# Kernel optimization log

Hardware: AMD Instinct MI355X
Metric: run time of the kernel (lower is better)

## Reference

```python
import jax, jax.numpy as jnp
import numpy as np

BITS = 4
MAXQ = (1 << BITS) - 1  # 15
GROUPSIZE = 128
IN_F = 8192
OUT_F = 8192
PACK = 32 // BITS  # 8 values per int32


def setup_inputs() -> dict:
    key = jax.random.key(0)
    k_x, k_w, k_z, k_s, k_b = jax.random.split(key, 5)
    groups = IN_F // GROUPSIZE
    x = jax.random.normal(k_x, (4, 32, IN_F), dtype=jnp.float32)
    # bit-packed int32 weight / zeros (random bit patterns are valid quantized data)
    qweight = jax.random.randint(k_w, (IN_F // PACK, OUT_F), 0, 2**31 - 1, dtype=jnp.int32)
    qzeros = jax.random.randint(k_z, (groups, OUT_F // PACK), 0, 2**31 - 1, dtype=jnp.int32)
    scales = (jax.random.uniform(k_s, (groups, OUT_F), dtype=jnp.float32) * 0.01 + 1e-3)
    g_idx = (jnp.arange(IN_F, dtype=jnp.int32) // GROUPSIZE).astype(jnp.int32)
    bias = jax.random.normal(k_b, (OUT_F,), dtype=jnp.float32) * 0.01
    return {"x": x, "qweight": qweight, "qzeros": qzeros, "scales": scales,
            "g_idx": g_idx, "bias": bias}


def _dequant(qweight, qzeros, scales, g_idx):
    shifts = jnp.arange(0, 32, BITS, dtype=jnp.int32)  # [PACK]
    # unpack weights along the input dim: [in/PACK, PACK, out] -> [in, out]
    w = (qweight[:, None, :] >> shifts[None, :, None]) & MAXQ
    w = w.reshape(-1, qweight.shape[1])
    # unpack zeros along the output dim: [groups, out/PACK, PACK] -> [groups, out]
    # GPTQ stores (zero - 1), so add 1 back
    z = ((qzeros[:, :, None] >> shifts[None, None, :]) & MAXQ) + 1
    z = z.reshape(qzeros.shape[0], -1)
    # per-group dequant: W[i, o] = scales[g_idx[i], o] * (w[i, o] - z[g_idx[i], o])
    W = scales[g_idx] * (w.astype(scales.dtype) - z[g_idx].astype(scales.dtype))
    return W  # [in, out]


def reference(x, qweight, qzeros, scales, g_idx, bias):
    W = _dequant(qweight, qzeros, scales, g_idx)
    out = jnp.einsum('bsi,io->bso', x, W) + bias
    return out
```

## Files before the change

### kernel.cpp

```cpp
#include <hip/hip_runtime.h>
#include <hip/hip_bf16.h>
#include <stdint.h>


#define IN_F 8192
#define OUT_F 8192
#define MROWS 128
#define KSPLIT 8
#define KCHUNK (IN_F / KSPLIT)
#define BN 64
#define BK 64

typedef short short8_t __attribute__((ext_vector_type(8)));
typedef float float4_t __attribute__((ext_vector_type(4)));

__device__ __forceinline__ void gl_lds16(const void* g, void* l) {
  auto g1 = (const __attribute__((address_space(1))) unsigned int*)((uintptr_t)g);
  auto l3 = (__attribute__((address_space(3))) unsigned int*)((uintptr_t)l);
  __builtin_amdgcn_global_load_lds(g1, l3, 16, 0, 0);
}

__global__ void cvt_x(const float* __restrict__ x, unsigned short* __restrict__ xb) {
  const int i = (blockIdx.x * 256 + threadIdx.x) * 8;
  float4_t a = *(const float4_t*)(x + i);
  float4_t b = *(const float4_t*)(x + i + 4);
  union { short8_t v; __hip_bfloat162 h[4]; } u;
  u.h[0] = __float22bfloat162_rn(make_float2(a.x, a.y));
  u.h[1] = __float22bfloat162_rn(make_float2(a.z, a.w));
  u.h[2] = __float22bfloat162_rn(make_float2(b.x, b.y));
  u.h[3] = __float22bfloat162_rn(make_float2(b.z, b.w));
  *(short8_t*)(xb + i) = u.v;
}

__global__ void init_out(float* __restrict__ out, const float* __restrict__ bias) {
  const int i = (blockIdx.x * 256 + threadIdx.x) * 4;
  const int o = i & (OUT_F - 1);
  *(float4_t*)(out + i) = *(const float4_t*)(bias + o);
}

__global__ __launch_bounds__(256, 4) void gptq_gemm(
    const unsigned short* __restrict__ xb,
    const int* __restrict__ qweight,
    const int* __restrict__ qzeros,
    const float* __restrict__ scales,
    float* __restrict__ out)
{
  __shared__ unsigned short As[MROWS * BK];
  __shared__ unsigned short Bs[BN * BK];

  const int tid  = threadIdx.x;
  const int lane = tid & 63;
  const int wv   = tid >> 6;
  const int wm   = (wv >> 1) * 64;
  const int wn   = (wv & 1) * 32;

  const int o0  = blockIdx.x * BN;
  const int kc0 = blockIdx.y * KCHUNK;

  const int a_kb = (lane & 7) ^ (lane >> 3);

  const int u = tid & 31;
  const int r = tid >> 5;

  float4_t acc[4][2];
  const float4_t z4 = {0.f, 0.f, 0.f, 0.f};
#pragma unroll
  for (int i = 0; i < 4; ++i)
#pragma unroll
    for (int j = 0; j < 2; ++j) acc[i][j] = z4;

  float sc[2], zs[2];
  {
    const int g = kc0 >> 7;
#pragma unroll
    for (int oi = 0; oi < 2; ++oi) {
      const int o = o0 + u + 32 * oi;
      sc[oi] = scales[g * OUT_F + o];
      const int zp = qzeros[g * (OUT_F / 8) + (o >> 3)];
      zs[oi] = sc[oi] * (float)(((zp >> (4 * (o & 7))) & 15) + 1);
    }
  }
  int qw[2];
  {
    const int kp = kc0 >> 3;
    qw[0] = qweight[(size_t)(kp + r) * OUT_F + o0 + u];
    qw[1] = qweight[(size_t)(kp + r) * OUT_F + o0 + u + 32];
  }

#pragma unroll 2
  for (int it = 0; it < KCHUNK / BK; ++it) {
    const int k0 = kc0 + it * BK;

#pragma unroll
    for (int inst = 0; inst < 4; ++inst) {
      const int mrow = wv * 32 + inst * 8 + (lane >> 3);
      gl_lds16(xb + (size_t)mrow * IN_F + k0 + a_kb * 8,
               (void*)(As + wv * 2048 + inst * 512));
    }

#pragma unroll
    for (int oi = 0; oi < 2; ++oi) {
      const int n = u + 32 * oi;
      union { short8_t v; __hip_bfloat162 h[4]; } bw;
#pragma unroll
      for (int jj = 0; jj < 4; ++jj) {
        const int w0 = (qw[oi] >> (8 * jj)) & 15;
        const int w1 = (qw[oi] >> (8 * jj + 4)) & 15;
        bw.h[jj] = __float22bfloat162_rn(make_float2(
            (float)w0 * sc[oi] - zs[oi], (float)w1 * sc[oi] - zs[oi]));
      }
      *(short8_t*)(Bs + n * BK + (r ^ (n & 7)) * 8) = bw.v;
    }

    __syncthreads();

    {
      const int itn = (it + 1 < KCHUNK / BK) ? it + 1 : it;
      const int kp = (kc0 + itn * BK) >> 3;
      qw[0] = qweight[(size_t)(kp + r) * OUT_F + o0 + u];
      qw[1] = qweight[(size_t)(kp + r) * OUT_F + o0 + u + 32];
      if ((((it + 1) & 1) == 0) && (it + 1 < KCHUNK / BK)) {
        const int g = (kc0 + (it + 1) * BK) >> 7;
#pragma unroll
        for (int oi = 0; oi < 2; ++oi) {
          const int o = o0 + u + 32 * oi;
          sc[oi] = scales[g * OUT_F + o];
          const int zp = qzeros[g * (OUT_F / 8) + (o >> 3)];
          zs[oi] = sc[oi] * (float)(((zp >> (4 * (o & 7))) & 15) + 1);
        }
      }
    }

#pragma unroll
    for (int ks = 0; ks < 2; ++ks) {
      const int c = ks * 4 + (lane >> 4);
      const int pos8 = (c ^ (lane & 7)) * 8;
      const int l15 = lane & 15;
      short8_t af[4], bf[2];
#pragma unroll
      for (int t = 0; t < 4; ++t)
        af[t] = *(const short8_t*)(As + (wm + t * 16 + l15) * BK + pos8);
#pragma unroll
      for (int t = 0; t < 2; ++t)
        bf[t] = *(const short8_t*)(Bs + (wn + t * 16 + l15) * BK + pos8);
#pragma unroll
      for (int mt = 0; mt < 4; ++mt)
#pragma unroll
        for (int nt = 0; nt < 2; ++nt)
          acc[mt][nt] = __builtin_amdgcn_mfma_f32_16x16x32_bf16(
              af[mt], bf[nt], acc[mt][nt], 0, 0, 0);
    }

    __syncthreads();
  }

  const int row4 = (lane >> 4) * 4;
  const int col = lane & 15;
#pragma unroll
  for (int mt = 0; mt < 4; ++mt)
#pragma unroll
    for (int nt = 0; nt < 2; ++nt)
#pragma unroll
      for (int rr = 0; rr < 4; ++rr) {
        const int m = wm + mt * 16 + row4 + rr;
        const int o = o0 + wn + nt * 16 + col;
        atomicAdd(out + (size_t)m * OUT_F + o, acc[mt][nt][rr]);
      }
}

extern "C" void kernel_launch(void* const* d_in, const int* in_sizes, int n_in,
                              void* d_out, int out_size, void* d_ws, size_t ws_size,
                              hipStream_t stream) {
  const float* x        = (const float*)d_in[0];
  const int*   qweight  = (const int*)d_in[1];
  const int*   qzeros   = (const int*)d_in[2];
  const float* scales   = (const float*)d_in[3];
  const float* bias     = (const float*)d_in[5];
  float* out = (float*)d_out;
  unsigned short* xb = (unsigned short*)d_ws;

  cvt_x<<<dim3((MROWS * IN_F) / (256 * 8)), 256, 0, stream>>>(x, xb);
  init_out<<<dim3((MROWS * OUT_F) / (256 * 4)), 256, 0, stream>>>(out, bias);
  gptq_gemm<<<dim3(OUT_F / BN, KSPLIT), 256, 0, stream>>>(xb, qweight, qzeros, scales, out);
}
```

Baseline: 130.0 us.

## Dequantize weights directly into MFMA B-fragments in registers, dropping B LDS tile

Each wave now loads its own packed weights in MFMA fragment order and dequantizes them straight into registers, so the B shared-memory tile and its store/load round trip go away. BK grows to 128 to match the group size, so scales and zeros are loaded once per iteration, and the A tile swizzle is reworked for the wider row. Dequant work is duplicated across the two waves that share each column slice, qweight loads are no longer prefetched across iterations, and the A LDS tile doubles in size, which may lower occupancy.

```diff
diff --git a/kernel.cpp b/kernel.cpp
--- a/kernel.cpp
+++ b/kernel.cpp
@@ -9,7 +9,7 @@
 #define KSPLIT 8
 #define KCHUNK (IN_F / KSPLIT)
 #define BN 64
-#define BK 64
+#define BK 128
 
 typedef short short8_t __attribute__((ext_vector_type(8)));
 typedef float float4_t __attribute__((ext_vector_type(4)));
@@ -46,21 +46,17 @@
     float* __restrict__ out)
 {
   __shared__ unsigned short As[MROWS * BK];
-  __shared__ unsigned short Bs[BN * BK];
 
   const int tid  = threadIdx.x;
   const int lane = tid & 63;
+  const int l15  = lane & 15;
+  const int qtr  = lane >> 4;
   const int wv   = tid >> 6;
   const int wm   = (wv >> 1) * 64;
   const int wn   = (wv & 1) * 32;
 
   const int o0  = blockIdx.x * BN;
   const int kc0 = blockIdx.y * KCHUNK;
-
-  const int a_kb = (lane & 7) ^ (lane >> 3);
-
-  const int u = tid & 31;
-  const int r = tid >> 5;
 
   float4_t acc[4][2];
   const float4_t z4 = {0.f, 0.f, 0.f, 0.f};
@@ -69,80 +65,72 @@
 #pragma unroll
     for (int j = 0; j < 2; ++j) acc[i][j] = z4;
 
-  float sc[2], zs[2];
-  {
-    const int g = kc0 >> 7;
-#pragma unroll
-    for (int oi = 0; oi < 2; ++oi) {
-      const int o = o0 + u + 32 * oi;
-      sc[oi] = scales[g * OUT_F + o];
-      const int zp = qzeros[g * (OUT_F / 8) + (o >> 3)];
-      zs[oi] = sc[oi] * (float)(((zp >> (4 * (o & 7))) & 15) + 1);
-    }
-  }
-  int qw[2];
-  {
-    const int kp = kc0 >> 3;
-    qw[0] = qweight[(size_t)(kp + r) * OUT_F + o0 + u];
-    qw[1] = qweight[(size_t)(kp + r) * OUT_F + o0 + u + 32];
-  }
-
 #pragma unroll 2
   for (int it = 0; it < KCHUNK / BK; ++it) {
     const int k0 = kc0 + it * BK;
+    const int g  = k0 >> 7;
 
+    int qw[4][2];
+    const int kp0 = k0 >> 3;
 #pragma unroll
-    for (int inst = 0; inst < 4; ++inst) {
-      const int mrow = wv * 32 + inst * 8 + (lane >> 3);
-      gl_lds16(xb + (size_t)mrow * IN_F + k0 + a_kb * 8,
-               (void*)(As + wv * 2048 + inst * 512));
+    for (int ks = 0; ks < 4; ++ks)
+#pragma unroll
+      for (int nt = 0; nt < 2; ++nt)
+        qw[ks][nt] = qweight[(size_t)(kp0 + ks * 4 + qtr) * OUT_F + o0 + wn + nt * 16 + l15];
+
+    float sc[2]; int zq[2];
+#pragma unroll
+    for (int nt = 0; nt < 2; ++nt) {
+      const int o = o0 + wn + nt * 16 + l15;
+      sc[nt] = scales[g * OUT_F + o];
+      zq[nt] = qzeros[g * (OUT_F / 8) + (o >> 3)];
     }
 
 #pragma unroll
-    for (int oi = 0; oi < 2; ++oi) {
-      const int n = u + 32 * oi;
-      union { short8_t v; __hip_bfloat162 h[4]; } bw;
-#pragma unroll
-      for (int jj = 0; jj < 4; ++jj) {
-        const int w0 = (qw[oi] >> (8 * jj)) & 15;
-        const int w1 = (qw[oi] >> (8 * jj + 4)) & 15;
-        bw.h[jj] = __float22bfloat162_rn(make_float2(
-            (float)w0 * sc[oi] - zs[oi], (float)w1 * sc[oi] - zs[oi]));
-      }
-      *(short8_t*)(Bs + n * BK + (r ^ (n & 7)) * 8) = bw.v;
+    for (int inst = 0; inst < 8; ++inst) {
+      const int m = wv * 32 + inst * 4 + (lane >> 4);
+      const int kb = (lane & 15) ^ (m & 15);
+      gl_lds16(xb + (size_t)m * IN_F + k0 + kb * 8,
+               (void*)(As + (wv * 32 + inst * 4) * BK));
     }
 
     __syncthreads();
 
-    {
-      const int itn = (it + 1 < KCHUNK / BK) ? it + 1 : it;
-      const int kp = (kc0 + itn * BK) >> 3;
-      qw[0] = qweight[(size_t)(kp + r) * OUT_F + o0 + u];
-      qw[1] = qweight[(size_t)(kp + r) * OUT_F + o0 + u + 32];
-      if ((((it + 1) & 1) == 0) && (it + 1 < KCHUNK / BK)) {
-        const int g = (kc0 + (it + 1) * BK) >> 7;
+    float zb[2];
 #pragma unroll
-        for (int oi = 0; oi < 2; ++oi) {
-          const int o = o0 + u + 32 * oi;
-          sc[oi] = scales[g * OUT_F + o];
-          const int zp = qzeros[g * (OUT_F / 8) + (o >> 3)];
-          zs[oi] = sc[oi] * (float)(((zp >> (4 * (o & 7))) & 15) + 1);
-        }
-      }
+    for (int nt = 0; nt < 2; ++nt) {
+      const int o = o0 + wn + nt * 16 + l15;
+      const int z = ((zq[nt] >> (4 * (o & 7))) & 15) + 1;
+      zb[nt] = -sc[nt] * (float)z;
     }
 
 #pragma unroll
-    for (int ks = 0; ks < 2; ++ks) {
-      const int c = ks * 4 + (lane >> 4);
-      const int pos8 = (c ^ (lane & 7)) * 8;
-      const int l15 = lane & 15;
-      short8_t af[4], bf[2];
+    for (int ks = 0; ks < 4; ++ks) {
+      const int c = ks * 4 + qtr;
+      const int pos8 = (c ^ l15) * 8;
+
+      short8_t af[4];
 #pragma unroll
       for (int t = 0; t < 4; ++t)
         af[t] = *(const short8_t*)(As + (wm + t * 16 + l15) * BK + pos8);
+
+      short8_t bf[2];
 #pragma unroll
-      for (int t = 0; t < 2; ++t)
-        bf[t] = *(const short8_t*)(Bs + (wn + t * 16 + l15) * BK + pos8);
+      for (int nt = 0; nt < 2; ++nt) {
+        union { short8_t v; __hip_bfloat162 h[4]; } bw;
+        const int q = qw[ks][nt];
+        const unsigned qe = (unsigned)q & 0x0F0F0F0Fu;
+        const unsigned qo = ((unsigned)q >> 4) & 0x0F0F0F0Fu;
+#pragma unroll
+        for (int jj = 0; jj < 4; ++jj) {
+          const float f0 = (float)((qe >> (8 * jj)) & 0xffu);
+          const float f1 = (float)((qo >> (8 * jj)) & 0xffu);
+          bw.h[jj] = __float22bfloat162_rn(make_float2(
+              fmaf(sc[nt], f0, zb[nt]), fmaf(sc[nt], f1, zb[nt])));
+        }
+        bf[nt] = bw.v;
+      }
+
 #pragma unroll
       for (int mt = 0; mt < 4; ++mt)
 #pragma unroll
@@ -155,7 +143,6 @@
   }
 
   const int row4 = (lane >> 4) * 4;
-  const int col = lane & 15;
 #pragma unroll
   for (int mt = 0; mt < 4; ++mt)
 #pragma unroll
@@ -163,7 +150,7 @@
 #pragma unroll
       for (int rr = 0; rr < 4; ++rr) {
         const int m = wm + mt * 16 + row4 + rr;
-        const int o = o0 + wn + nt * 16 + col;
+        const int o = o0 + wn + nt * 16 + l15;
         atomicAdd(out + (size_t)m * OUT_F + o, acc[mt][nt][rr]);
       }
 }
```

After: 128.1 us. About the same (-1.4%).
